# Performance work log

Hardware: AMD Instinct MI355X
Metric: run time of the kernel (lower is better)

Reference implementation:

```python
import jax, jax.numpy as jnp
import numpy as np

# norse LIFCell default constants
DT = 1e-3
TAU_SYN_INV = 200.0
TAU_MEM_INV = 100.0
V_TH = 1.0
ALPHA = 100.0  # SuperSpike surrogate slope
BN_EPS = 1e-5
DECAY = 0.995

@jax.custom_vjp
def spike_fn(x):
    return (x > 0).astype(x.dtype)

def _spike_fwd(x):
    return spike_fn(x), x

def _spike_bwd(x, g):
    return (g / (ALPHA * jnp.abs(x) + 1.0) ** 2,)

spike_fn.defvjp(_spike_fwd, _spike_bwd)

def bn(x, g, b, m, v):
    return (x - m) * jax.lax.rsqrt(v + BN_EPS) * g + b

def lif_step(inp, v, i):
    # explicit Euler LIF update (v_leak = v_reset = 0)
    v_dec = v + DT * TAU_MEM_INV * (-v + i)
    i_dec = i * (1.0 - DT * TAU_SYN_INV)
    z = spike_fn(v_dec - V_TH)
    v_new = (1.0 - z) * v_dec
    i_new = i_dec + inp
    return z, v_new, i_new

def setup_inputs() -> dict:
    key = jax.random.key(0)
    ks = jax.random.split(key, 8)
    B, F, T = 2048, 512, 100
    H1, H2, H3, O = 1024, 512, 256, 2
    def xavier(k, fan_out, fan_in):
        lim = np.sqrt(6.0 / (fan_in + fan_out)).astype(np.float32)
        return jax.random.uniform(k, (fan_out, fan_in), jnp.float32, -lim, lim)
    def bn_params(k, n):
        return dict(g=jax.random.uniform(k, (n,), jnp.float32, 0.5, 1.5),
                    b=jnp.zeros((n,), jnp.float32),
                    m=jnp.zeros((n,), jnp.float32),
                    v=jnp.ones((n,), jnp.float32))
    bni = bn_params(ks[1], F); bn1 = bn_params(ks[2], H1)
    bn2 = bn_params(ks[3], H2); bn3 = bn_params(ks[4], H3)
    return {
        "x": jax.random.normal(ks[0], (B, F, T), jnp.float32),
        "bni_g": bni["g"], "bni_b": bni["b"], "bni_m": bni["m"], "bni_v": bni["v"],
        "W1": xavier(ks[5], H1, F), "b1": jnp.zeros((H1,), jnp.float32),
        "bn1_g": bn1["g"], "bn1_b": bn1["b"], "bn1_m": bn1["m"], "bn1_v": bn1["v"],
        "W2": xavier(ks[6], H2, H1), "b2": jnp.zeros((H2,), jnp.float32),
        "bn2_g": bn2["g"], "bn2_b": bn2["b"], "bn2_m": bn2["m"], "bn2_v": bn2["v"],
        "W3": xavier(ks[7], H3, H2), "b3": jnp.zeros((H3,), jnp.float32),
        "bn3_g": bn3["g"], "bn3_b": bn3["b"], "bn3_m": bn3["m"], "bn3_v": bn3["v"],
        "Wout": xavier(jax.random.fold_in(key, 99), O, H3),
        "bout": jnp.zeros((O,), jnp.float32),
    }

def reference(x, bni_g, bni_b, bni_m, bni_v,
              W1, b1, bn1_g, bn1_b, bn1_m, bn1_v,
              W2, b2, bn2_g, bn2_b, bn2_m, bn2_v,
              W3, b3, bn3_g, bn3_b, bn3_m, bn3_v,
              Wout, bout):
    B, F, T = x.shape
    O = Wout.shape[0]
    xs = jnp.moveaxis(x, 2, 0)  # (T, B, F)
    weights = DECAY ** jnp.arange(T - 1, -1, -1, dtype=x.dtype)  # (T,)

    def step(carry, inp):
        (v1, i1, v2, i2, v3, i3, vo, io, acc) = carry
        x_t, w = inp
        h = bn(x_t, bni_g, bni_b, bni_m, bni_v)
        c1 = bn(h @ W1.T + b1, bn1_g, bn1_b, bn1_m, bn1_v)
        z1, v1, i1 = lif_step(c1, v1, i1)
        c2 = bn(z1 @ W2.T + b2, bn2_g, bn2_b, bn2_m, bn2_v)
        z2, v2, i2 = lif_step(c2, v2, i2)
        c3 = bn(z2 @ W3.T + b3, bn3_g, bn3_b, bn3_m, bn3_v)
        z3, v3, i3 = lif_step(c3, v3, i3)
        co = z3 @ Wout.T + bout
        zo, vo, io = lif_step(co, vo, io)
        acc = acc + zo * w
        return (v1, i1, v2, i2, v3, i3, vo, io, acc), None

    zf = lambda n: jnp.zeros((B, n), x.dtype)
    init = (zf(W1.shape[0]), zf(W1.shape[0]), zf(W2.shape[0]), zf(W2.shape[0]),
            zf(W3.shape[0]), zf(W3.shape[0]), zf(O), zf(O), zf(O))
    carry, _ = jax.lax.scan(step, init, (xs, weights))
    return carry[-1]
```

## Files before the change

### kernel.cpp

```cpp
#include <hip/hip_runtime.h>
#include <cmath>

#define BATCH 2048
#define FDIM  512
#define TDIM  100
#define H1    1024
#define H2    512
#define H3    256
#define ODIM  2
#define M_ALL (TDIM * BATCH)

typedef __attribute__((ext_vector_type(8))) _Float16 f16x8;
typedef __attribute__((ext_vector_type(4))) _Float16 f16x4;
typedef __attribute__((ext_vector_type(4))) float f32x4;
typedef __attribute__((ext_vector_type(4))) int i32x4;

struct W100 { float w[TDIM]; };

__device__ __forceinline__ void gl16(const void* g, void* l) {
  __builtin_amdgcn_global_load_lds(
      (const __attribute__((address_space(1))) unsigned int*)g,
      (__attribute__((address_space(3))) unsigned int*)l, 16, 0, 0);
}

__device__ __forceinline__ void lif_update(float c, float& v, float& i, float& z) {
  float vd = v + 0.1f * (i - v);
  float id = 0.8f * i;
  z = (vd - 1.0f) > 0.0f ? 1.0f : 0.0f;
  v = (z != 0.0f) ? 0.0f : vd;
  i = id + c;
}

__global__ void zero_kernel(float* __restrict__ p, int n) {
  for (int i = blockIdx.x * blockDim.x + threadIdx.x; i < n; i += gridDim.x * blockDim.x)
    p[i] = 0.0f;
}

__global__ void tchunk_kernel(const float* __restrict__ x, _Float16* __restrict__ xp) {
  __shared__ float tile[64][105];
  const int f0 = blockIdx.x * 64;
  const int b  = blockIdx.y;
  const int tid = threadIdx.x;
  const size_t xb = (size_t)b * FDIM * TDIM;
  for (int idx = tid; idx < 1600; idx += 256) {
    const int f = idx / 25, q = idx % 25;
    float4 v = *reinterpret_cast<const float4*>(&x[xb + (size_t)(f0 + f) * TDIM + q * 4]);
    tile[f][q * 4 + 0] = v.x; tile[f][q * 4 + 1] = v.y;
    tile[f][q * 4 + 2] = v.z; tile[f][q * 4 + 3] = v.w;
  }
  __syncthreads();
  const size_t PS = (size_t)M_ALL * FDIM;
  for (int idx = tid; idx < 1600; idx += 256) {
    const int t = idx >> 4, fq = idx & 15;
    f16x4 h, m;
    #pragma unroll
    for (int j = 0; j < 4; ++j) {
      float xa = tile[fq * 4 + j][t] * 64.0f;
      _Float16 hh = (_Float16)xa;
      float rm = (xa - (float)hh) * 4096.0f;
      h[j] = hh;
      m[j] = (_Float16)rm;
    }
    const size_t o = ((size_t)t * BATCH + b) * FDIM + f0 + fq * 4;
    *reinterpret_cast<f16x4*>(&xp[o])      = h;
    *reinterpret_cast<f16x4*>(&xp[PS + o]) = m;
  }
}

__global__ void fold1_f16(const float* __restrict__ W1, const float* __restrict__ b1,
                          const float* __restrict__ g1, const float* __restrict__ bb1,
                          const float* __restrict__ m1, const float* __restrict__ v1,
                          const float* __restrict__ gi, const float* __restrict__ bi,
                          const float* __restrict__ mi, const float* __restrict__ vi,
                          _Float16* __restrict__ W1p, float* __restrict__ s1,
                          float* __restrict__ e1) {
  __shared__ float swf[FDIM];
  __shared__ float red[8];
  __shared__ float bsw[1];
  const int j = blockIdx.x, tid = threadIdx.x;
  const float sg = g1[j] / sqrtf(v1[j] + 1e-5f);
  float part = 0.0f, pmax = 0.0f;
  for (int f = tid; f < FDIM; f += 256) {
    float si = gi[f] / sqrtf(vi[f] + 1e-5f);
    float h0 = bi[f] - mi[f] * si;
    float w  = W1[j * FDIM + f];
    part += w * h0;
    float wf = w * si * sg;
    swf[f] = wf;
    pmax = fmaxf(pmax, fabsf(wf));
  }
  #pragma unroll
  for (int s = 1; s < 64; s <<= 1) {
    part += __shfl_xor(part, s);
    pmax = fmaxf(pmax, __shfl_xor(pmax, s));
  }
  if ((tid & 63) == 0) { red[tid >> 6] = part; red[4 + (tid >> 6)] = pmax; }
  __syncthreads();
  if (tid == 0) {
    float d = red[0] + red[1] + red[2] + red[3];
    e1[j] = (d + b1[j] - m1[j]) * sg + bb1[j];
    float mx = fmaxf(fmaxf(red[4], red[5]), fmaxf(red[6], red[7]));
    int e = 0;
    if (mx > 0.0f) frexpf(mx, &e);
    s1[j] = exp2f((float)(e - 11));
    bsw[0] = exp2f((float)(5 - e));
  }
  __syncthreads();
  const float SW = bsw[0];
  const size_t PS = (size_t)H1 * FDIM;
  for (int f = tid; f < FDIM; f += 256) {
    float wa = swf[f] * SW;
    _Float16 wh = (_Float16)wa;
    float r = (wa - (float)wh) * 4096.0f;
    W1p[(size_t)j * FDIM + f]      = wh;
    W1p[PS + (size_t)j * FDIM + f] = (_Float16)r;
  }
}

__global__ void foldS_i8(const float* __restrict__ W, const float* __restrict__ b,
                         const float* __restrict__ g, const float* __restrict__ bb,
                         const float* __restrict__ m, const float* __restrict__ v,
                         signed char* __restrict__ Wq, float* __restrict__ qs,
                         float* __restrict__ e, int N, int K) {
  __shared__ float swf[1024];
  __shared__ float red[4];
  __shared__ int bse[1];
  const int j = blockIdx.x, tid = threadIdx.x;
  const float sg = g[j] / sqrtf(v[j] + 1e-5f);
  float pmax = 0.0f;
  for (int k = tid; k < K; k += 256) {
    float wf = W[(size_t)j * K + k] * sg;
    swf[k] = wf;
    pmax = fmaxf(pmax, fabsf(wf));
  }
  #pragma unroll
  for (int s = 1; s < 64; s <<= 1) pmax = fmaxf(pmax, __shfl_xor(pmax, s));
  if ((tid & 63) == 0) red[tid >> 6] = pmax;
  __syncthreads();
  if (tid == 0) {
    float mx = fmaxf(fmaxf(red[0], red[1]), fmaxf(red[2], red[3]));
    int ee = 0;
    if (mx > 0.0f) frexpf(mx, &ee);
    qs[j] = exp2f((float)(ee - 27));
    bse[0] = 27 - ee;
    e[j] = (b[j] - m[j]) * sg + bb[j];
  }
  __syncthreads();
  const double sc = ldexp(1.0, bse[0]);
  const size_t PS = (size_t)N * K;
  for (int k = tid; k < K; k += 256) {
    long D = llround((double)swf[k] * sc);
    #pragma unroll
    for (int p = 0; p < 3; p++) {
      int d = (int)(D & 127);
      if (d >= 64) d -= 128;
      Wq[(size_t)p * PS + (size_t)j * K + k] = (signed char)d;
      D = (D - d) >> 7;
    }
    Wq[3 * PS + (size_t)j * K + k] = (signed char)D;
  }
}

__global__ __launch_bounds__(256, 2)
void g1c_kernel(const _Float16* __restrict__ A, const _Float16* __restrict__ Wp,
                const float* __restrict__ s1, const float* __restrict__ e1,
                float* __restrict__ cOut)
{
  constexpr int BM = 128, BN = 64, K = FDIM, N = H1, BK = 64;
  constexpr int FR = 4, FC = 2, WTM = 64, WTN = 32;
  __shared__ __align__(16) _Float16 As[2][BM][BK];
  __shared__ __align__(16) _Float16 Bs[2][BN][BK];
  const int tid = threadIdx.x, lane = tid & 63, wid = tid >> 6;
  const int wr = wid >> 1, wc = wid & 1;
  const int l16 = lane & 15, lq = lane >> 4;
  const int bnk = blockIdx.x, bmk = blockIdx.y;
  const size_t APS = (size_t)M_ALL * FDIM;
  const size_t WPS = (size_t)N * K;
  const int lrow8 = lane >> 3, lslot = lane & 7;

  f32x4 accA[FR][FC] = {}, accB[FR][FC] = {};

  auto stage = [&](int it) {
    const int k0 = it * BK;
    #pragma unroll
    for (int q = 0; q < 8; ++q) {
      int i = q * 4 + wid;
      int s = i >> 4, r0 = (i & 15) * 8;
      int row = r0 + lrow8;
      int ss = lslot ^ (row & 7);
      gl16(A + (size_t)s * APS + (size_t)(bmk * BM + row) * K + k0 + ss * 8, &As[s][r0][0]);
    }
    #pragma unroll
    for (int q = 0; q < 4; ++q) {
      int i = q * 4 + wid;
      int s = i >> 3, r0 = (i & 7) * 8;
      int row = r0 + lrow8;
      int ss = lslot ^ (row & 7);
      gl16(Wp + (size_t)s * WPS + (size_t)(bnk * BN + row) * K + k0 + ss * 8, &Bs[s][r0][0]);
    }
  };

  auto loadA = [&](int kh, int s, int fr) -> f16x8 {
    int row = wr * WTM + fr * 16 + l16;
    int slot = ((kh << 2) | lq) ^ (row & 7);
    return *reinterpret_cast<const f16x8*>(&As[s][row][slot * 8]);
  };
  auto loadB = [&](int kh, int s, int fc) -> f16x8 {
    int row = wc * WTN + fc * 16 + l16;
    int slot = ((kh << 2) | lq) ^ (row & 7);
    return *reinterpret_cast<const f16x8*>(&Bs[s][row][slot * 8]);
  };

  stage(0);
  __syncthreads();
  constexpr int NK = K / BK;
  for (int it = 0; it < NK; ++it) {
    {
      f16x8 af[2][FR], bf[2][FC];
      #pragma unroll
      for (int s = 0; s < 2; ++s) {
        #pragma unroll
        for (int fr = 0; fr < FR; ++fr) af[s][fr] = loadA(0, s, fr);
        #pragma unroll
        for (int fc = 0; fc < FC; ++fc) bf[s][fc] = loadB(0, s, fc);
      }
      #pragma unroll
      for (int fr = 0; fr < FR; ++fr)
        #pragma unroll
        for (int fc = 0; fc < FC; ++fc) {
          accA[fr][fc] = __builtin_amdgcn_mfma_f32_16x16x32_f16(af[0][fr], bf[0][fc], accA[fr][fc], 0, 0, 0);
          accB[fr][fc] = __builtin_amdgcn_mfma_f32_16x16x32_f16(af[0][fr], bf[1][fc], accB[fr][fc], 0, 0, 0);
          accB[fr][fc] = __builtin_amdgcn_mfma_f32_16x16x32_f16(af[1][fr], bf[0][fc], accB[fr][fc], 0, 0, 0);
        }
    }
    {
      f16x8 af[2][FR], bf[2][FC];
      #pragma unroll
      for (int s = 0; s < 2; ++s) {
        #pragma unroll
        for (int fr = 0; fr < FR; ++fr) af[s][fr] = loadA(1, s, fr);
        #pragma unroll
        for (int fc = 0; fc < FC; ++fc) bf[s][fc] = loadB(1, s, fc);
      }
      __syncthreads();
      if (it + 1 < NK) stage(it + 1);
      #pragma unroll
      for (int fr = 0; fr < FR; ++fr)
        #pragma unroll
        for (int fc = 0; fc < FC; ++fc) {
          accA[fr][fc] = __builtin_amdgcn_mfma_f32_16x16x32_f16(af[0][fr], bf[0][fc], accA[fr][fc], 0, 0, 0);
          accB[fr][fc] = __builtin_amdgcn_mfma_f32_16x16x32_f16(af[0][fr], bf[1][fc], accB[fr][fc], 0, 0, 0);
          accB[fr][fc] = __builtin_amdgcn_mfma_f32_16x16x32_f16(af[1][fr], bf[0][fc], accB[fr][fc], 0, 0, 0);
        }
      __syncthreads();
    }
  }

  #pragma unroll
  for (int fc = 0; fc < FC; ++fc) {
    const int n = bnk * BN + wc * WTN + fc * 16 + l16;
    const float eb = e1[n], sn = s1[n];
    #pragma unroll
    for (int fr = 0; fr < FR; ++fr) {
      const int row0 = bmk * BM + wr * WTM + fr * 16 + lq * 4;
      #pragma unroll
      for (int r = 0; r < 4; ++r)
        cOut[(size_t)(row0 + r) * N + n] =
            sn * (accA[fr][fc][r] + 0.000244140625f * accB[fr][fc][r]) + eb;
    }
  }
}

template<int BM, int BN>
__global__ __launch_bounds__(256, 2)
void gSc_kernel(const signed char* __restrict__ A, const signed char* __restrict__ Wq,
                const float* __restrict__ qs, const float* __restrict__ eb_,
                float* __restrict__ cOut, const int N, const int K)
{
  constexpr int BKI = 128;
  constexpr int WTM = BM / 2, WTN = BN / 2, FR = WTM / 16, FC = WTN / 16;
  constexpr int RA = BM / 8, RB = BN / 8;
  __shared__ __align__(16) signed char As[BM][BKI];
  __shared__ __align__(16) signed char Bs[4][BN][BKI];
  const int tid = threadIdx.x, lane = tid & 63, wid = tid >> 6;
  const int wr = wid >> 1, wc = wid & 1;
  const int l16 = lane & 15, lq = lane >> 4;
  const int bnk = blockIdx.x, bmk = blockIdx.y;
  const size_t WPS = (size_t)N * K;
  const int lrow8 = lane >> 3, lslot = lane & 7;

  i32x4 acc[4][FR][FC] = {};

  auto stage = [&](int it) {
    const int k0 = it * BKI;
    #pragma unroll
    for (int q = 0; q < RA / 4; ++q) {
      int i = q * 4 + wid;
      int r0 = i * 8, row = r0 + lrow8;
      int ss = lslot ^ (row & 7);
      gl16(A + (size_t)(bmk * BM + row) * K + k0 + ss * 16, &As[r0][0]);
    }
    #pragma unroll
    for (int q = 0; q < RB; ++q) {
      int i = q * 4 + wid;
      int s = i / RB, r0 = (i % RB) * 8, row = r0 + lrow8;
      int ss = lslot ^ (row & 7);
      gl16(Wq + (size_t)s * WPS + (size_t)(bnk * BN + row) * K + k0 + ss * 16, &Bs[s][r0][0]);
    }
  };

  auto loadA = [&](int kh, int fr) -> i32x4 {
    int row = wr * WTM + fr * 16 + l16;
    int slot = ((kh << 2) | lq) ^ (row & 7);
    return *reinterpret_cast<const i32x4*>(&As[row][slot * 16]);
  };
  auto loadB = [&](int kh, int s, int fc) -> i32x4 {
    int row = wc * WTN + fc * 16 + l16;
    int slot = ((kh << 2) | lq) ^ (row & 7);
    return *reinterpret_cast<const i32x4*>(&Bs[s][row][slot * 16]);
  };

  stage(0);
  __syncthreads();
  const int NK = K / BKI;
  for (int it = 0; it < NK; ++it) {
    {
      i32x4 av[FR], bv[4][FC];
      #pragma unroll
      for (int fr = 0; fr < FR; ++fr) av[fr] = loadA(0, fr);
      #pragma unroll
      for (int s = 0; s < 4; ++s)
        #pragma unroll
        for (int fc = 0; fc < FC; ++fc) bv[s][fc] = loadB(0, s, fc);
      #pragma unroll
      for (int s = 0; s < 4; ++s)
        #pragma unroll
        for (int fr = 0; fr < FR; ++fr)
          #pragma unroll
          for (int fc = 0; fc < FC; ++fc)
            acc[s][fr][fc] = __builtin_amdgcn_mfma_i32_16x16x64_i8(av[fr], bv[s][fc], acc[s][fr][fc], 0, 0, 0);
    }
    {
      i32x4 av[FR], bv[4][FC];
      #pragma unroll
      for (int fr = 0; fr < FR; ++fr) av[fr] = loadA(1, fr);
      #pragma unroll
      for (int s = 0; s < 4; ++s)
        #pragma unroll
        for (int fc = 0; fc < FC; ++fc) bv[s][fc] = loadB(1, s, fc);
      __syncthreads();
      if (it + 1 < NK) stage(it + 1);
      #pragma unroll
      for (int s = 0; s < 4; ++s)
        #pragma unroll
        for (int fr = 0; fr < FR; ++fr)
          #pragma unroll
          for (int fc = 0; fc < FC; ++fc)
            acc[s][fr][fc] = __builtin_amdgcn_mfma_i32_16x16x64_i8(av[fr], bv[s][fc], acc[s][fr][fc], 0, 0, 0);
      __syncthreads();
    }
  }

  #pragma unroll
  for (int fc = 0; fc < FC; ++fc) {
    const int n = bnk * BN + wc * WTN + fc * 16 + l16;
    const float qv = qs[n], eb = eb_[n];
    #pragma unroll
    for (int fr = 0; fr < FR; ++fr) {
      const int row0 = bmk * BM + wr * WTM + fr * 16 + lq * 4;
      #pragma unroll
      for (int r = 0; r < 4; ++r) {
        int slo = acc[0][fr][fc][r] + (acc[1][fr][fc][r] << 7) + (acc[2][fr][fc][r] << 14);
        cOut[(size_t)(row0 + r) * N + n] =
            qv * fmaf(2097152.0f, (float)acc[3][fr][fc][r], (float)slo) + eb;
      }
    }
  }
}

__global__ void scan_lif_kernel(const float* __restrict__ c, signed char* __restrict__ z,
                                int NN)
{
  const int i4 = (blockIdx.x * 256 + threadIdx.x) * 4;
  float4 v  = make_float4(0.f, 0.f, 0.f, 0.f);
  float4 ii = make_float4(0.f, 0.f, 0.f, 0.f);
  for (int t = 0; t < TDIM; ++t) {
    const size_t o = (size_t)t * NN + i4;
    float4 cc = *reinterpret_cast<const float4*>(&c[o]);
    float4 zz;
    lif_update(cc.x, v.x, ii.x, zz.x);
    lif_update(cc.y, v.y, ii.y, zz.y);
    lif_update(cc.z, v.z, ii.z, zz.z);
    lif_update(cc.w, v.w, ii.w, zz.w);
    unsigned pz = (zz.x != 0.f ? 1u : 0u) | (zz.y != 0.f ? 256u : 0u)
                | (zz.z != 0.f ? 65536u : 0u) | (zz.w != 0.f ? 16777216u : 0u);
    *reinterpret_cast<unsigned*>(&z[o]) = pz;
  }
}

__global__ void scan3out_kernel(const float* __restrict__ c3,
                                const float* __restrict__ Wout, const float* __restrict__ bout,
                                float* __restrict__ out, W100 wts)
{
  const int lane = threadIdx.x & 63, wv = threadIdx.x >> 6;
  const int b = blockIdx.x * 4 + wv;
  const int n0 = lane * 4;
  float4 v  = make_float4(0.f, 0.f, 0.f, 0.f);
  float4 ii = make_float4(0.f, 0.f, 0.f, 0.f);
  const float4 w0 = *reinterpret_cast<const float4*>(&Wout[n0]);
  const float4 w1 = *reinterpret_cast<const float4*>(&Wout[H3 + n0]);
  const float bo0 = bout[0], bo1 = bout[1];
  float vo0 = 0.f, io0 = 0.f, vo1 = 0.f, io1 = 0.f;
  float acc0 = 0.0f, acc1 = 0.0f;
  for (int t = 0; t < TDIM; ++t) {
    const size_t o = ((size_t)t * BATCH + b) * H3 + n0;
    float4 cc = *reinterpret_cast<const float4*>(&c3[o]);
    float4 zz;
    lif_update(cc.x, v.x, ii.x, zz.x);
    lif_update(cc.y, v.y, ii.y, zz.y);
    lif_update(cc.z, v.z, ii.z, zz.z);
    lif_update(cc.w, v.w, ii.w, zz.w);
    float s0 = fmaf(zz.x, w0.x, fmaf(zz.y, w0.y, fmaf(zz.z, w0.z, zz.w * w0.w)));
    float s1 = fmaf(zz.x, w1.x, fmaf(zz.y, w1.y, fmaf(zz.z, w1.z, zz.w * w1.w)));
    #pragma unroll
    for (int m = 1; m < 64; m <<= 1) {
      s0 += __shfl_xor(s0, m);
      s1 += __shfl_xor(s1, m);
    }
    float zo0, zo1;
    lif_update(s0 + bo0, vo0, io0, zo0);
    lif_update(s1 + bo1, vo1, io1, zo1);
    acc0 += zo0 * wts.w[t];
    acc1 += zo1 * wts.w[t];
  }
  if (lane == 0) {
    const int oidx = b * ODIM;
    out[oidx]     = acc0;
    out[oidx + 1] = acc1;
  }
}

__global__ void fold1_kernel(const float* __restrict__ W1, const float* __restrict__ b1,
                             const float* __restrict__ g1, const float* __restrict__ bb1,
                             const float* __restrict__ m1, const float* __restrict__ v1,
                             const float* __restrict__ gi, const float* __restrict__ bi,
                             const float* __restrict__ mi, const float* __restrict__ vi,
                             float* __restrict__ W1f, float* __restrict__ e1) {
  const int j = blockIdx.x;
  const int tid = threadIdx.x;
  const float sg = g1[j] / sqrtf(v1[j] + 1e-5f);
  float part = 0.0f;
  for (int f = tid; f < FDIM; f += 256) {
    float si = gi[f] / sqrtf(vi[f] + 1e-5f);
    float h0 = bi[f] - mi[f] * si;
    float w  = W1[j * FDIM + f];
    part += w * h0;
    W1f[j * FDIM + f] = w * si * sg;
  }
  #pragma unroll
  for (int m = 1; m < 64; m <<= 1) part += __shfl_xor(part, m);
  __shared__ float red[4];
  if ((tid & 63) == 0) red[tid >> 6] = part;
  __syncthreads();
  if (tid == 0) {
    float d = red[0] + red[1] + red[2] + red[3];
    e1[j] = (d + b1[j] - m1[j]) * sg + bb1[j];
  }
}

__global__ void foldS_kernel(const float* __restrict__ W, const float* __restrict__ b,
                             const float* __restrict__ g, const float* __restrict__ bb,
                             const float* __restrict__ m, const float* __restrict__ v,
                             float* __restrict__ Wf, float* __restrict__ e, int K) {
  const int j = blockIdx.x;
  const float sg = g[j] / sqrtf(v[j] + 1e-5f);
  for (int k = threadIdx.x; k < K; k += 256)
    Wf[j * K + k] = W[j * K + k] * sg;
  if (threadIdx.x == 0) e[j] = (b[j] - m[j]) * sg + bb[j];
}

template<int TM, int TN, bool CONTIG>
__global__ __launch_bounds__(256, 2)
void gemm_lif_kernel(const float* __restrict__ A, size_t ars, size_t acs,
                     const float* __restrict__ W, const float* __restrict__ ebias,
                     float* __restrict__ vst, float* __restrict__ ist,
                     float* __restrict__ zout, int N, int K)
{
  constexpr int BK = 16;
  constexpr int BM = 16 * TM;
  constexpr int BN = 16 * TN;
  __shared__ float As[BK][BM];
  __shared__ float Bs[BK][BN];
  const int tid = threadIdx.x;
  const int tx = tid & 15, ty = tid >> 4;
  const int bn = blockIdx.x, bm = blockIdx.y;
  const float* Ablk = A + (size_t)bm * BM * ars;
  const float* Wblk = W + (size_t)bn * BN * (size_t)K;

  float acc[TM][TN];
  #pragma unroll
  for (int r = 0; r < TM; r++)
    #pragma unroll
    for (int c = 0; c < TN; c++) acc[r][c] = 0.0f;

  for (int k0 = 0; k0 < K; k0 += BK) {
    if (CONTIG) {
      constexpr int A4 = BM * BK / 4;
      #pragma unroll
      for (int q = 0; q < A4 / 256; q++) {
        int idx = q * 256 + tid;
        int r = idx >> 2;
        int kq = (idx & 3) << 2;
        float4 val = *reinterpret_cast<const float4*>(Ablk + (size_t)r * ars + (size_t)(k0 + kq));
        As[kq + 0][r] = val.x; As[kq + 1][r] = val.y;
        As[kq + 2][r] = val.z; As[kq + 3][r] = val.w;
      }
    } else {
      #pragma unroll
      for (int q = 0; q < BM * BK / 256; q++) {
        int idx = q * 256 + tid;
        int r = idx >> 4;
        int kk = idx & 15;
        As[kk][r] = Ablk[(size_t)r * ars + (size_t)(k0 + kk) * acs];
      }
    }
    {
      int n  = tid >> 2;
      int kq = (tid & 3) << 2;
      float4 val = *reinterpret_cast<const float4*>(Wblk + (size_t)n * K + (size_t)(k0 + kq));
      Bs[kq + 0][n] = val.x; Bs[kq + 1][n] = val.y;
      Bs[kq + 2][n] = val.z; Bs[kq + 3][n] = val.w;
    }
    __syncthreads();
    #pragma unroll
    for (int kk = 0; kk < BK; kk++) {
      float a[TM], bv[TN];
      const float4* ap = reinterpret_cast<const float4*>(&As[kk][ty * TM]);
      *reinterpret_cast<float4*>(&a[0]) = ap[0];
      if (TM == 8) *reinterpret_cast<float4*>(&a[4]) = ap[1];
      *reinterpret_cast<float4*>(&bv[0]) = *reinterpret_cast<const float4*>(&Bs[kk][tx * TN]);
      #pragma unroll
      for (int r = 0; r < TM; r++)
        #pragma unroll
        for (int c = 0; c < TN; c++)
          acc[r][c] = fmaf(a[r], bv[c], acc[r][c]);
    }
    __syncthreads();
  }

  const int n0 = bn * BN + tx * TN;
  const float4 ev = *reinterpret_cast<const float4*>(ebias + n0);
  #pragma unroll
  for (int r = 0; r < TM; r++) {
    const int brow = bm * BM + ty * TM + r;
    const size_t idx = (size_t)brow * N + n0;
    float c0 = acc[r][0] + ev.x;
    float c1 = acc[r][1] + ev.y;
    float c2 = acc[r][2] + ev.z;
    float c3 = acc[r][3] + ev.w;
    float4 vv = *reinterpret_cast<const float4*>(vst + idx);
    float4 ii = *reinterpret_cast<const float4*>(ist + idx);
    float4 zz;
    lif_update(c0, vv.x, ii.x, zz.x);
    lif_update(c1, vv.y, ii.y, zz.y);
    lif_update(c2, vv.z, ii.z, zz.z);
    lif_update(c3, vv.w, ii.w, zz.w);
    *reinterpret_cast<float4*>(zout + idx) = zz;
    *reinterpret_cast<float4*>(vst  + idx) = vv;
    *reinterpret_cast<float4*>(ist  + idx) = ii;
  }
}

__global__ void out_kernel(const float* __restrict__ z3, const float* __restrict__ Wout,
                           const float* __restrict__ bout, float* __restrict__ vo,
                           float* __restrict__ io, float* __restrict__ acc, float wt) {
  const int idx = blockIdx.x * 256 + threadIdx.x;
  if (idx >= BATCH * ODIM) return;
  const int b = idx >> 1, o = idx & 1;
  const float4* zr = reinterpret_cast<const float4*>(z3 + (size_t)b * H3);
  const float4* wr = reinterpret_cast<const float4*>(Wout + o * H3);
  float s = 0.0f;
  #pragma unroll 4
  for (int k = 0; k < H3 / 4; k++) {
    float4 zv = zr[k], wv = wr[k];
    s += zv.x * wv.x + zv.y * wv.y + zv.z * wv.z + zv.w * wv.w;
  }
  float cin = s + bout[o];
  float v = vo[idx], i = io[idx], z;
  lif_update(cin, v, i, z);
  vo[idx] = v; io[idx] = i;
  acc[idx] += z * wt;
}

extern "C" void kernel_launch(void* const* d_in, const int* in_sizes, int n_in,
                              void* d_out, int out_size, void* d_ws, size_t ws_size,
                              hipStream_t stream) {
  const float* x     = (const float*)d_in[0];
  const float* bni_g = (const float*)d_in[1];
  const float* bni_b = (const float*)d_in[2];
  const float* bni_m = (const float*)d_in[3];
  const float* bni_v = (const float*)d_in[4];
  const float* W1    = (const float*)d_in[5];
  const float* b1    = (const float*)d_in[6];
  const float* bn1_g = (const float*)d_in[7];
  const float* bn1_b = (const float*)d_in[8];
  const float* bn1_m = (const float*)d_in[9];
  const float* bn1_v = (const float*)d_in[10];
  const float* W2    = (const float*)d_in[11];
  const float* b2    = (const float*)d_in[12];
  const float* bn2_g = (const float*)d_in[13];
  const float* bn2_b = (const float*)d_in[14];
  const float* bn2_m = (const float*)d_in[15];
  const float* bn2_v = (const float*)d_in[16];
  const float* W3    = (const float*)d_in[17];
  const float* b3    = (const float*)d_in[18];
  const float* bn3_g = (const float*)d_in[19];
  const float* bn3_b = (const float*)d_in[20];
  const float* bn3_m = (const float*)d_in[21];
  const float* bn3_v = (const float*)d_in[22];
  const float* Wout  = (const float*)d_in[23];
  const float* bout  = (const float*)d_in[24];
  float* out = (float*)d_out;

  float* ws = (float*)d_ws;
  size_t off = 0;
  auto alloc = [&](size_t n) { float* p = ws + off; off += n; return p; };

  float* e1 = alloc(H1);
  float* e2 = alloc(H2);
  float* e3 = alloc(H3);
  float* s1 = alloc(H1);
  float* q2 = alloc(H2);
  float* q3 = alloc(H3);
  unsigned char* base = (unsigned char*)(ws + off);
  size_t boff = 0;
  auto carve = [&](size_t bytes) {
    void* p = base + boff;
    boff += (bytes + 255) & ~(size_t)255;
    return p;
  };
  _Float16* W1p   = (_Float16*)carve((size_t)2 * H1 * FDIM * 2);
  signed char* W2q = (signed char*)carve((size_t)4 * H2 * H1);
  signed char* W3q = (signed char*)carve((size_t)4 * H3 * H2);
  signed char* z1  = (signed char*)carve((size_t)M_ALL * H1);
  signed char* z2  = (signed char*)carve((size_t)M_ALL * H2);
  void* regionA = carve((size_t)2 * M_ALL * FDIM * 2);
  void* regionB = carve((size_t)M_ALL * H1 * 4);
  _Float16* Xp = (_Float16*)regionA;
  float* c2    = (float*)regionA;
  float* c1    = (float*)regionB;
  float* c3    = (float*)regionB;
  const size_t needed = off * sizeof(float) + boff;

  if (ws_size >= needed) {
    fold1_f16<<<H1, 256, 0, stream>>>(W1, b1, bn1_g, bn1_b, bn1_m, bn1_v,
                                      bni_g, bni_b, bni_m, bni_v, W1p, s1, e1);
    foldS_i8<<<H2, 256, 0, stream>>>(W2, b2, bn2_g, bn2_b, bn2_m, bn2_v, W2q, q2, e2, H2, H1);
    foldS_i8<<<H3, 256, 0, stream>>>(W3, b3, bn3_g, bn3_b, bn3_m, bn3_v, W3q, q3, e3, H3, H2);

    tchunk_kernel<<<dim3(FDIM / 64, BATCH), 256, 0, stream>>>(x, Xp);
    g1c_kernel<<<dim3(H1 / 64, M_ALL / 128), 256, 0, stream>>>(Xp, W1p, s1, e1, c1);
    scan_lif_kernel<<<BATCH * H1 / 1024, 256, 0, stream>>>(c1, z1, BATCH * H1);
    gSc_kernel<64, 64><<<dim3(H2 / 64, M_ALL / 64), 256, 0, stream>>>(z1, W2q, q2, e2, c2, H2, H1);
    scan_lif_kernel<<<BATCH * H2 / 1024, 256, 0, stream>>>(c2, z2, BATCH * H2);
    gSc_kernel<64, 32><<<dim3(H3 / 32, M_ALL / 64), 256, 0, stream>>>(z2, W3q, q3, e3, c3, H3, H2);
    W100 wts;
    for (int t = 0; t < TDIM; ++t)
      wts.w[t] = (float)std::pow(0.995, (double)(TDIM - 1 - t));
    scan3out_kernel<<<BATCH / 4, 256, 0, stream>>>(c3, Wout, bout, out, wts);
    return;
  }

  off = 0;
  float* W1f = alloc((size_t)H1 * FDIM);
  float* W2f = alloc((size_t)H2 * H1);
  float* W3f = alloc((size_t)H3 * H2);
  float* fe1 = alloc(H1);
  float* fe2 = alloc(H2);
  float* fe3 = alloc(H3);
  float* fv1 = alloc((size_t)BATCH * H1);
  float* fi1 = alloc((size_t)BATCH * H1);
  float* fv2 = alloc((size_t)BATCH * H2);
  float* fi2 = alloc((size_t)BATCH * H2);
  float* fv3 = alloc((size_t)BATCH * H3);
  float* fi3 = alloc((size_t)BATCH * H3);
  float* fvo = alloc((size_t)BATCH * ODIM);
  float* fio = alloc((size_t)BATCH * ODIM);
  float* fz1 = alloc((size_t)BATCH * H1);
  float* fz2 = alloc((size_t)BATCH * H2);
  float* fz3 = alloc((size_t)BATCH * H3);

  const int nstate = BATCH * (2 * H1 + 2 * H2 + 2 * H3 + 2 * ODIM);
  zero_kernel<<<2048, 256, 0, stream>>>(fv1, nstate);
  zero_kernel<<<16, 256, 0, stream>>>(out, BATCH * ODIM);

  fold1_kernel<<<H1, 256, 0, stream>>>(W1, b1, bn1_g, bn1_b, bn1_m, bn1_v,
                                       bni_g, bni_b, bni_m, bni_v, W1f, fe1);
  foldS_kernel<<<H2, 256, 0, stream>>>(W2, b2, bn2_g, bn2_b, bn2_m, bn2_v, W2f, fe2, H1);
  foldS_kernel<<<H3, 256, 0, stream>>>(W3, b3, bn3_g, bn3_b, bn3_m, bn3_v, W3f, fe3, H2);

  const dim3 fg1(H1 / 64, BATCH / 128);
  const dim3 fg2(H2 / 64, BATCH / 64);
  const dim3 fg3(H3 / 64, BATCH / 64);

  for (int t = 0; t < TDIM; t++) {
    gemm_lif_kernel<8, 4, false><<<fg1, 256, 0, stream>>>(
        x + t, (size_t)FDIM * TDIM, TDIM, W1f, fe1, fv1, fi1, fz1, H1, FDIM);
    gemm_lif_kernel<4, 4, true><<<fg2, 256, 0, stream>>>(fz1, H1, 1, W2f, fe2, fv2, fi2, fz2, H2, H1);
    gemm_lif_kernel<4, 4, true><<<fg3, 256, 0, stream>>>(fz2, H2, 1, W3f, fe3, fv3, fi3, fz3, H3, H2);
    float wt = (float)std::pow(0.995, (double)(TDIM - 1 - t));
    out_kernel<<<BATCH * ODIM / 256, 256, 0, stream>>>(fz3, Wout, bout, fvo, fio, out, wt);
  }
}
```

Before: 1.972 ms.

## Store GEMM A-operands in K-chunked layout and swizzle block order for XCD locality

```diff
diff --git a/kernel.cpp b/kernel.cpp
--- a/kernel.cpp
+++ b/kernel.cpp
@@ -38,7 +38,8 @@
 
 __global__ void tchunk_kernel(const float* __restrict__ x, _Float16* __restrict__ xp) {
   __shared__ float tile[64][105];
-  const int f0 = blockIdx.x * 64;
+  const int kt = blockIdx.x;
+  const int f0 = kt * 64;
   const int b  = blockIdx.y;
   const int tid = threadIdx.x;
   const size_t xb = (size_t)b * FDIM * TDIM;
@@ -61,7 +62,7 @@
       h[j] = hh;
       m[j] = (_Float16)rm;
     }
-    const size_t o = ((size_t)t * BATCH + b) * FDIM + f0 + fq * 4;
+    const size_t o = ((size_t)kt * M_ALL + (size_t)t * BATCH + b) * 64 + fq * 4;
     *reinterpret_cast<f16x4*>(&xp[o])      = h;
     *reinterpret_cast<f16x4*>(&xp[PS + o]) = m;
   }
@@ -161,7 +162,7 @@
   }
 }
 
-__global__ __launch_bounds__(256, 2)
+__global__ __launch_bounds__(256, 3)
 void g1c_kernel(const _Float16* __restrict__ A, const _Float16* __restrict__ Wp,
                 const float* __restrict__ s1, const float* __restrict__ e1,
                 float* __restrict__ cOut)
@@ -173,7 +174,9 @@
   const int tid = threadIdx.x, lane = tid & 63, wid = tid >> 6;
   const int wr = wid >> 1, wc = wid & 1;
   const int l16 = lane & 15, lq = lane >> 4;
-  const int bnk = blockIdx.x, bmk = blockIdx.y;
+  const int chunk = gridDim.x >> 3;
+  const int flat = (blockIdx.x & 7) * chunk + (blockIdx.x >> 3);
+  const int bnk = flat & 15, bmk = flat >> 4;
   const size_t APS = (size_t)M_ALL * FDIM;
   const size_t WPS = (size_t)N * K;
   const int lrow8 = lane >> 3, lslot = lane & 7;
@@ -181,15 +184,16 @@
   f32x4 accA[FR][FC] = {}, accB[FR][FC] = {};
 
   auto stage = [&](int it) {
-    const int k0 = it * BK;
     #pragma unroll
     for (int q = 0; q < 8; ++q) {
       int i = q * 4 + wid;
       int s = i >> 4, r0 = (i & 15) * 8;
       int row = r0 + lrow8;
       int ss = lslot ^ (row & 7);
-      gl16(A + (size_t)s * APS + (size_t)(bmk * BM + row) * K + k0 + ss * 8, &As[s][r0][0]);
-    }
+      gl16(A + (size_t)s * APS + ((size_t)it * M_ALL + (size_t)(bmk * BM + row)) * 64 + ss * 8,
+           &As[s][r0][0]);
+    }
+    const int k0 = it * BK;
     #pragma unroll
     for (int q = 0; q < 4; ++q) {
       int i = q * 4 + wid;
@@ -272,7 +276,7 @@
 }
 
 template<int BM, int BN>
-__global__ __launch_bounds__(256, 2)
+__global__ __launch_bounds__(256, 3)
 void gSc_kernel(const signed char* __restrict__ A, const signed char* __restrict__ Wq,
                 const float* __restrict__ qs, const float* __restrict__ eb_,
                 float* __restrict__ cOut, const int N, const int K)
@@ -285,21 +289,23 @@
   const int tid = threadIdx.x, lane = tid & 63, wid = tid >> 6;
   const int wr = wid >> 1, wc = wid & 1;
   const int l16 = lane & 15, lq = lane >> 4;
-  const int bnk = blockIdx.x, bmk = blockIdx.y;
+  const int chunk = gridDim.x >> 3;
+  const int flat = (blockIdx.x & 7) * chunk + (blockIdx.x >> 3);
+  const int bnk = flat & 7, bmk = flat >> 3;
   const size_t WPS = (size_t)N * K;
   const int lrow8 = lane >> 3, lslot = lane & 7;
 
   i32x4 acc[4][FR][FC] = {};
 
   auto stage = [&](int it) {
-    const int k0 = it * BKI;
     #pragma unroll
     for (int q = 0; q < RA / 4; ++q) {
       int i = q * 4 + wid;
       int r0 = i * 8, row = r0 + lrow8;
       int ss = lslot ^ (row & 7);
-      gl16(A + (size_t)(bmk * BM + row) * K + k0 + ss * 16, &As[r0][0]);
-    }
+      gl16(A + ((size_t)it * M_ALL + (size_t)(bmk * BM + row)) * BKI + ss * 16, &As[r0][0]);
+    }
+    const int k0 = it * BKI;
     #pragma unroll
     for (int q = 0; q < RB; ++q) {
       int i = q * 4 + wid;
@@ -379,9 +385,13 @@
 }
 
 __global__ void scan_lif_kernel(const float* __restrict__ c, signed char* __restrict__ z,
-                                int NN)
+                                int H)
 {
+  const int NN = BATCH * H;
   const int i4 = (blockIdx.x * 256 + threadIdx.x) * 4;
+  const int b = i4 / H, n = i4 % H;
+  const size_t zb = (size_t)(n >> 7) * M_ALL;
+  const int nw = n & 127;
   float4 v  = make_float4(0.f, 0.f, 0.f, 0.f);
   float4 ii = make_float4(0.f, 0.f, 0.f, 0.f);
   for (int t = 0; t < TDIM; ++t) {
@@ -394,7 +404,7 @@
     lif_update(cc.w, v.w, ii.w, zz.w);
     unsigned pz = (zz.x != 0.f ? 1u : 0u) | (zz.y != 0.f ? 256u : 0u)
                 | (zz.z != 0.f ? 65536u : 0u) | (zz.w != 0.f ? 16777216u : 0u);
-    *reinterpret_cast<unsigned*>(&z[o]) = pz;
+    *reinterpret_cast<unsigned*>(&z[(zb + (size_t)t * BATCH + b) * 128 + nw]) = pz;
   }
 }
 
@@ -659,11 +669,11 @@
     foldS_i8<<<H3, 256, 0, stream>>>(W3, b3, bn3_g, bn3_b, bn3_m, bn3_v, W3q, q3, e3, H3, H2);
 
     tchunk_kernel<<<dim3(FDIM / 64, BATCH), 256, 0, stream>>>(x, Xp);
-    g1c_kernel<<<dim3(H1 / 64, M_ALL / 128), 256, 0, stream>>>(Xp, W1p, s1, e1, c1);
-    scan_lif_kernel<<<BATCH * H1 / 1024, 256, 0, stream>>>(c1, z1, BATCH * H1);
-    gSc_kernel<64, 64><<<dim3(H2 / 64, M_ALL / 64), 256, 0, stream>>>(z1, W2q, q2, e2, c2, H2, H1);
-    scan_lif_kernel<<<BATCH * H2 / 1024, 256, 0, stream>>>(c2, z2, BATCH * H2);
-    gSc_kernel<64, 32><<<dim3(H3 / 32, M_ALL / 64), 256, 0, stream>>>(z2, W3q, q3, e3, c3, H3, H2);
+    g1c_kernel<<<(H1 / 64) * (M_ALL / 128), 256, 0, stream>>>(Xp, W1p, s1, e1, c1);
+    scan_lif_kernel<<<BATCH * H1 / 1024, 256, 0, stream>>>(c1, z1, H1);
+    gSc_kernel<64, 64><<<(H2 / 64) * (M_ALL / 64), 256, 0, stream>>>(z1, W2q, q2, e2, c2, H2, H1);
+    scan_lif_kernel<<<BATCH * H2 / 1024, 256, 0, stream>>>(c2, z2, H2);
+    gSc_kernel<64, 32><<<(H3 / 32) * (M_ALL / 64), 256, 0, stream>>>(z2, W3q, q3, e3, c3, H3, H2);
     W100 wts;
     for (int t = 0; t < TDIM; ++t)
       wts.w[t] = (float)std::pow(0.995, (double)(TDIM - 1 - t));
```

New measurement: 1.852 ms. 6.1% less time.
